# Kernel optimization log

Hardware: AMD Instinct MI355X
Metric: run time of the kernel (lower is better)

The kernel has to match this reference:

```python
import jax, jax.numpy as jnp
import numpy as np

EPS = 1e-10


def setup_inputs() -> dict:
    key = jax.random.key(0)
    k1, k2 = jax.random.split(key)
    B, F, T = 64, 80, 8000
    x = jax.random.normal(k1, (B, F, T), dtype=jnp.float32)
    # relative lengths in [0.5, 1.0] so every sample has plenty of valid frames
    lengths = 0.5 + 0.5 * jax.random.uniform(k2, (B,), dtype=jnp.float32)
    return {"x": x, "lengths": lengths}


def reference(x, lengths):
    # x: [B, F, T]; lengths: [B] relative fractions of valid time steps.
    B, F, T = x.shape
    n = jnp.round(lengths * T).astype(jnp.int32)            # valid frames per sample [B]
    mask = (jnp.arange(T)[None, :] < n[:, None])            # [B, T]
    mask = mask[:, None, :].astype(x.dtype)                 # [B, 1, T]
    nf = n.astype(x.dtype)[:, None, None]                   # [B, 1, 1]
    # per-sample, per-feature mean over valid frames (torch.mean over dim=1 of [F,T_valid])
    mean = jnp.sum(x * mask, axis=2, keepdims=True) / nf    # [B, F, 1]
    # torch.std default: unbiased (ddof=1)
    var = jnp.sum(jnp.square((x - mean) * mask), axis=2, keepdims=True) / (nf - 1.0)
    std = jnp.maximum(jnp.sqrt(var), EPS)                   # [B, F, 1]
    # normalization is applied to ALL frames (including padding), matching the original
    return (x - mean) / std
```

## Files before the change

### kernel.cpp

```cpp
#include <hip/hip_runtime.h>
#include <hip/hip_bf16.h>
#include <math.h>


#define ROW_T 8000
#define TV (ROW_T / 4)
#define BLOCK 256
#define VPT 8
#define EPS 1e-10f

__device__ __forceinline__ float block_reduce_sum(float v, float* lds) {
    #pragma unroll
    for (int off = 32; off > 0; off >>= 1)
        v += __shfl_down(v, off, 64);
    const int wave = threadIdx.x >> 6;
    const int lane = threadIdx.x & 63;
    if (lane == 0) lds[wave] = v;
    __syncthreads();
    float r = (lds[0] + lds[1]) + (lds[2] + lds[3]);
    __syncthreads();
    return r;
}

__global__ __launch_bounds__(BLOCK) void isn_kernel(
        const float* __restrict__ x,
        const float* __restrict__ lengths,
        float* __restrict__ out,
        int F) {
    __shared__ float lds[4];

    const int row = blockIdx.x;
    const int b = row / F;
    const float* __restrict__ xr = x + (size_t)row * ROW_T;
    float* __restrict__ outr = out + (size_t)row * ROW_T;
    const int tid = threadIdx.x;

    const int n = (int)rintf(lengths[b] * (float)ROW_T);
    const float nf = (float)n;

    float4 v[VPT];
    #pragma unroll
    for (int it = 0; it < VPT; ++it) {
        const int idx = tid + it * BLOCK;
        if (idx < TV) v[it] = ((const float4*)xr)[idx];
    }

    float s = 0.0f;
    #pragma unroll
    for (int it = 0; it < VPT; ++it) {
        const int base = (tid + it * BLOCK) * 4;
        if (base < ROW_T) {
            s += (base + 0 < n) ? v[it].x : 0.0f;
            s += (base + 1 < n) ? v[it].y : 0.0f;
            s += (base + 2 < n) ? v[it].z : 0.0f;
            s += (base + 3 < n) ? v[it].w : 0.0f;
        }
    }
    const float mean = block_reduce_sum(s, lds) / nf;

    float ss = 0.0f;
    #pragma unroll
    for (int it = 0; it < VPT; ++it) {
        const int base = (tid + it * BLOCK) * 4;
        if (base < ROW_T) {
            float dx = v[it].x - mean, dy = v[it].y - mean;
            float dz = v[it].z - mean, dw = v[it].w - mean;
            ss += (base + 0 < n) ? dx * dx : 0.0f;
            ss += (base + 1 < n) ? dy * dy : 0.0f;
            ss += (base + 2 < n) ? dz * dz : 0.0f;
            ss += (base + 3 < n) ? dw * dw : 0.0f;
        }
    }
    const float var = block_reduce_sum(ss, lds) / (nf - 1.0f);
    const float stdv = fmaxf(sqrtf(var), EPS);
    const float inv = 1.0f / stdv;

    #pragma unroll
    for (int it = 0; it < VPT; ++it) {
        const int idx = tid + it * BLOCK;
        if (idx < TV) {
            float4 o;
            o.x = (v[it].x - mean) * inv;
            o.y = (v[it].y - mean) * inv;
            o.z = (v[it].z - mean) * inv;
            o.w = (v[it].w - mean) * inv;
            ((float4*)outr)[idx] = o;
        }
    }
}

extern "C" void kernel_launch(void* const* d_in, const int* in_sizes, int n_in,
                              void* d_out, int out_size, void* d_ws, size_t ws_size,
                              hipStream_t stream) {
    const float* x = (const float*)d_in[0];
    const float* lengths = (const float*)d_in[1];
    float* out = (float*)d_out;

    const int B = in_sizes[1];
    const int F = in_sizes[0] / (B * ROW_T);
    const int rows = B * F;

    isn_kernel<<<rows, BLOCK, 0, stream>>>(x, lengths, out, F);
}
```

Measured before the change: 280.1 us.

## Fuse mean and variance into one-pass reduction with nontemporal IO and 512-thread blocks

Computes sum and sum of squares in a single pass and merges the two block reductions into one shuffle plus LDS exchange, removing a barrier round and the second sweep over registers. Loads and stores use nontemporal hints, and the block grows to 512 threads with 4 float4 per thread. The one-pass variance formula risks cancellation error compared with the two-pass version, though for near zero-mean data this is small.

After: 265.5 us. 5.2% less time.

```diff
diff --git a/kernel.cpp b/kernel.cpp
--- a/kernel.cpp
+++ b/kernel.cpp
@@ -5,73 +5,65 @@
 
 #define ROW_T 8000
 #define TV (ROW_T / 4)
-#define BLOCK 256
-#define VPT 8
+#define BLOCK 512
+#define WAVES (BLOCK / 64)
+#define VPT 4
 #define EPS 1e-10f
 
-__device__ __forceinline__ float block_reduce_sum(float v, float* lds) {
-    #pragma unroll
-    for (int off = 32; off > 0; off >>= 1)
-        v += __shfl_down(v, off, 64);
-    const int wave = threadIdx.x >> 6;
-    const int lane = threadIdx.x & 63;
-    if (lane == 0) lds[wave] = v;
-    __syncthreads();
-    float r = (lds[0] + lds[1]) + (lds[2] + lds[3]);
-    __syncthreads();
-    return r;
-}
+typedef float v4f __attribute__((ext_vector_type(4)));
 
 __global__ __launch_bounds__(BLOCK) void isn_kernel(
         const float* __restrict__ x,
         const float* __restrict__ lengths,
         float* __restrict__ out,
         int F) {
-    __shared__ float lds[4];
+    __shared__ float2 lds[WAVES];
 
     const int row = blockIdx.x;
     const int b = row / F;
-    const float* __restrict__ xr = x + (size_t)row * ROW_T;
-    float* __restrict__ outr = out + (size_t)row * ROW_T;
+    const v4f* __restrict__ xr = (const v4f*)(x + (size_t)row * ROW_T);
+    v4f* __restrict__ outr = (v4f*)(out + (size_t)row * ROW_T);
     const int tid = threadIdx.x;
 
     const int n = (int)rintf(lengths[b] * (float)ROW_T);
     const float nf = (float)n;
 
-    float4 v[VPT];
+    v4f v[VPT];
     #pragma unroll
     for (int it = 0; it < VPT; ++it) {
         const int idx = tid + it * BLOCK;
-        if (idx < TV) v[it] = ((const float4*)xr)[idx];
+        if (idx < TV) v[it] = __builtin_nontemporal_load(&xr[idx]);
     }
 
-    float s = 0.0f;
+    float s = 0.0f, ss = 0.0f;
     #pragma unroll
     for (int it = 0; it < VPT; ++it) {
         const int base = (tid + it * BLOCK) * 4;
         if (base < ROW_T) {
-            s += (base + 0 < n) ? v[it].x : 0.0f;
-            s += (base + 1 < n) ? v[it].y : 0.0f;
-            s += (base + 2 < n) ? v[it].z : 0.0f;
-            s += (base + 3 < n) ? v[it].w : 0.0f;
+            #pragma unroll
+            for (int j = 0; j < 4; ++j) {
+                const float xv = (base + j < n) ? v[it][j] : 0.0f;
+                s += xv;
+                ss = fmaf(xv, xv, ss);
+            }
         }
     }
-    const float mean = block_reduce_sum(s, lds) / nf;
 
-    float ss = 0.0f;
     #pragma unroll
-    for (int it = 0; it < VPT; ++it) {
-        const int base = (tid + it * BLOCK) * 4;
-        if (base < ROW_T) {
-            float dx = v[it].x - mean, dy = v[it].y - mean;
-            float dz = v[it].z - mean, dw = v[it].w - mean;
-            ss += (base + 0 < n) ? dx * dx : 0.0f;
-            ss += (base + 1 < n) ? dy * dy : 0.0f;
-            ss += (base + 2 < n) ? dz * dz : 0.0f;
-            ss += (base + 3 < n) ? dw * dw : 0.0f;
-        }
+    for (int off = 32; off > 0; off >>= 1) {
+        s  += __shfl_down(s, off, 64);
+        ss += __shfl_down(ss, off, 64);
     }
-    const float var = block_reduce_sum(ss, lds) / (nf - 1.0f);
+    const int wave = tid >> 6;
+    const int lane = tid & 63;
+    if (lane == 0) lds[wave] = make_float2(s, ss);
+    __syncthreads();
+    float rs = 0.0f, rss = 0.0f;
+    #pragma unroll
+    for (int i = 0; i < WAVES; ++i) { rs += lds[i].x; rss += lds[i].y; }
+
+    const float mean = rs / nf;
+    const float var = (rss - rs * rs / nf) / (nf - 1.0f);
     const float stdv = fmaxf(sqrtf(var), EPS);
     const float inv = 1.0f / stdv;
 
@@ -79,12 +71,11 @@
     for (int it = 0; it < VPT; ++it) {
         const int idx = tid + it * BLOCK;
         if (idx < TV) {
-            float4 o;
-            o.x = (v[it].x - mean) * inv;
-            o.y = (v[it].y - mean) * inv;
-            o.z = (v[it].z - mean) * inv;
-            o.w = (v[it].w - mean) * inv;
-            ((float4*)outr)[idx] = o;
+            v4f o;
+            #pragma unroll
+            for (int j = 0; j < 4; ++j)
+                o[j] = (v[it][j] - mean) * inv;
+            __builtin_nontemporal_store(o, &outr[idx]);
         }
     }
 }
```
